# Kernel tuning notes

Hardware: AMD Instinct MI355X
Metric: run time of the kernel (lower is better)

Reference implementation:

```python
import jax, jax.numpy as jnp
import numpy as np

N_NODES = 100000
N_EDGES = 1600000
NFEAT, NHID, NCLASS = 128, 64, 40


def setup_inputs() -> dict:
    key = jax.random.key(0)
    k = jax.random.split(key, 6)
    x = jax.random.normal(k[0], (N_NODES, NFEAT), dtype=jnp.float32)
    edge_index = jax.random.randint(k[1], (2, N_EDGES), 0, N_NODES, dtype=jnp.int64)
    edge_weight = jax.random.uniform(k[2], (N_EDGES,), dtype=jnp.float32)
    # Glorot-style init as in PyG GCNConv.reset_parameters
    W1 = jax.random.normal(k[3], (NFEAT, NHID), dtype=jnp.float32) * (1.0 / np.sqrt(NFEAT))
    b1 = jnp.zeros((NHID,), dtype=jnp.float32)
    W2 = jax.random.normal(k[4], (NHID, NCLASS), dtype=jnp.float32) * (1.0 / np.sqrt(NHID))
    b2 = jnp.zeros((NCLASS,), dtype=jnp.float32)
    return {"x": x, "edge_index": edge_index, "edge_weight": edge_weight,
            "W1": W1, "b1": b1, "W2": W2, "b2": b2}


def _gcn_conv(x, edge_index, edge_weight, W, b):
    """PyG GCNConv: add self-loops, symmetric gcn_norm, linear, scatter-add, bias."""
    n = x.shape[0]
    loop = jnp.arange(n)
    row = jnp.concatenate([edge_index[0], loop])  # source nodes
    col = jnp.concatenate([edge_index[1], loop])  # target nodes
    w = jnp.concatenate([edge_weight, jnp.ones((n,), edge_weight.dtype)])
    deg = jax.ops.segment_sum(w, col, num_segments=n)          # [N]
    dinv = jnp.where(deg > 0, jax.lax.rsqrt(deg), 0.0)
    norm = dinv[row] * w * dinv[col]                           # [E+N]
    h = x @ W                                                  # [N, out]
    msg = norm[:, None] * h[row]                               # gather: [E+N, out]
    out = jax.ops.segment_sum(msg, col, num_segments=n)        # scatter-add: [N, out]
    return out + b


def reference(x, edge_index, edge_weight, W1, b1, W2, b2):
    h = jax.nn.relu(_gcn_conv(x, edge_index, edge_weight, W1, b1))
    # F.dropout with training=False is identity (eval mode)
    return _gcn_conv(h, edge_index, edge_weight, W2, b2)
```

## Files before the change

kernel.cpp:

```cpp
#include <hip/hip_runtime.h>
#include <hip/hip_bf16.h>

#define N_NODES 100000
#define N_EDGES 1600000
#define NFEAT 128
#define NHID 64
#define NCLASS 40
#define CAP 64

#define BIN_SHIFT 9
#define BIN_NODES 512
#define NBIN ((N_NODES + BIN_NODES - 1) / BIN_NODES)
#define SCAP 10240
#define CHUNK 4096
#define EPT 16

using frag_ab = __attribute__((ext_vector_type(8))) short;
using frag_cd = __attribute__((ext_vector_type(4))) float;


__device__ __forceinline__ unsigned pack2(float a, float b) {
    unsigned ua = __float_as_uint(a), ub = __float_as_uint(b);
    unsigned ra = (ua + 0x7FFFu + ((ua >> 16) & 1u)) >> 16;
    unsigned rb = (ub + 0x7FFFu + ((ub >> 16) & 1u)) >> 16;
    return ra | (rb << 16);
}
__device__ __forceinline__ unsigned short bf16rtn(float f) {
    unsigned u = __float_as_uint(f);
    return (unsigned short)((u + 0x7FFFu + ((u >> 16) & 1u)) >> 16);
}
__device__ __forceinline__ float lo16(unsigned w) { return __uint_as_float(w << 16); }
__device__ __forceinline__ float hi16(unsigned w) { return __uint_as_float(w & 0xFFFF0000u); }


__global__ __launch_bounds__(256) void bin_kernel(const int* __restrict__ ei,
                                                  const float* __restrict__ ew,
                                                  int* __restrict__ bincnt,
                                                  uint2* __restrict__ staging) {
    __shared__ int lcnt[NBIN];
    __shared__ int gbase[NBIN];
    int t = threadIdx.x;
    for (int i = t; i < NBIN; i += 256) lcnt[i] = 0;
    __syncthreads();

    int base = blockIdx.x * CHUNK;
    int c[EPT]; unsigned en[EPT];
#pragma unroll
    for (int u = 0; u < EPT; ++u) {
        int e = base + u * 256 + t;
        if (e < N_EDGES) {
            c[u] = ei[N_EDGES + e];
            unsigned wq = (unsigned)fminf(ew[e] * 32768.0f, 32767.0f);
            en[u] = ((unsigned)ei[e] << 15) | wq;
        } else {
            c[u] = -1;
        }
    }
#pragma unroll
    for (int u = 0; u < EPT; ++u)
        if (c[u] >= 0) atomicAdd(&lcnt[c[u] >> BIN_SHIFT], 1);
    __syncthreads();
    if (t < NBIN) {
        int n = lcnt[t];
        gbase[t] = (n > 0) ? atomicAdd(&bincnt[t], n) : 0;
    }
    __syncthreads();
    if (t < NBIN) lcnt[t] = 0;
    __syncthreads();
#pragma unroll
    for (int u = 0; u < EPT; ++u) {
        if (c[u] >= 0) {
            int b = c[u] >> BIN_SHIFT;
            int p = gbase[b] + atomicAdd(&lcnt[b], 1);
            if (p < SCAP)
                staging[(size_t)b * SCAP + p] = make_uint2(en[u], (unsigned)c[u]);
        }
    }
}


__global__ __launch_bounds__(512) void place_kernel(const int* __restrict__ bincnt,
                                                    const uint2* __restrict__ staging,
                                                    unsigned* __restrict__ bucket,
                                                    int* __restrict__ cnt,
                                                    float* __restrict__ dinv) {
    __shared__ int lpos[BIN_NODES];
    __shared__ float lws[BIN_NODES];
    int b = blockIdx.x;
    int t = threadIdx.x;
    for (int i = t; i < BIN_NODES; i += 512) { lpos[i] = 0; lws[i] = 0.0f; }
    __syncthreads();

    int nodebase = b << BIN_SHIFT;
    int n = bincnt[b];
    if (n > SCAP) n = SCAP;
    const uint2* st = staging + (size_t)b * SCAP;
    for (int i = t; i < n; i += 512) {
        uint2 en = st[i];
        int local = (int)en.y - nodebase;
        int p = atomicAdd(&lpos[local], 1);
        if (p < CAP) bucket[((size_t)en.y << 6) + p] = en.x;
        atomicAdd(&lws[local], (float)(en.x & 32767u) * (1.0f / 32768.0f));
    }
    __syncthreads();
    for (int i = t; i < BIN_NODES; i += 512) {
        int node = nodebase + i;
        if (node < N_NODES) {
            cnt[node] = min(lpos[i], CAP);
            dinv[node] = rsqrtf(1.0f + lws[i]);
        }
    }
}


__global__ __launch_bounds__(256) void prep_kernel(const float* __restrict__ W1,
                                                   const float* __restrict__ W2,
                                                   unsigned short* __restrict__ w1t,
                                                   unsigned short* __restrict__ w2t) {
    int idx = blockIdx.x * 256 + threadIdx.x;
    if (idx < NFEAT * NHID) {
        int k = idx >> 6, n = idx & 63;
        w1t[n * NFEAT + k] = bf16rtn(W1[idx]);
    }
    int idx2 = idx - NFEAT * NHID;
    if (idx2 >= 0 && idx2 < NHID * NCLASS) {
        int k = idx2 / NCLASS, n = idx2 - k * NCLASS;
        w2t[n * NHID + k] = bf16rtn(W2[idx2]);
    }
}


__global__ __launch_bounds__(256) void gemm1_kernel(const float* __restrict__ x,
                                                    const unsigned short* __restrict__ w1t,
                                                    unsigned short* __restrict__ h1b) {
    __shared__ unsigned short sm[16384];
    int t = threadIdx.x;
    int row0 = blockIdx.x * 64;

#pragma unroll
    for (int p = 0; p < 4; ++p) {
        int id = p * 256 + t;
        int r = id >> 4;
        int c = id & 15;
        int gr = row0 + r; if (gr > N_NODES - 1) gr = N_NODES - 1;
        const float* src = x + (size_t)gr * NFEAT + c * 8;
        float4 f0 = *(const float4*)src;
        float4 f1 = *(const float4*)(src + 4);
        uint4 pk = make_uint4(pack2(f0.x, f0.y), pack2(f0.z, f0.w),
                              pack2(f1.x, f1.y), pack2(f1.z, f1.w));
        int cs = c ^ (r & 15);
        *(uint4*)(&sm[r * 128 + cs * 8]) = pk;
    }
    const uint4* wt4 = (const uint4*)w1t;
#pragma unroll
    for (int p = 0; p < 4; ++p) {
        int id = p * 256 + t;
        int n = id >> 4;
        int c = id & 15;
        uint4 v = wt4[id];
        int cs = c ^ (n & 15);
        *(uint4*)(&sm[8192 + n * 128 + cs * 8]) = v;
    }
    __syncthreads();

    int w = t >> 6, l = t & 63;
    int li = l & 15, q = l >> 4;
    int arow = w * 16 + li;

    frag_cd acc0 = {0.f, 0.f, 0.f, 0.f};
    frag_cd acc1 = {0.f, 0.f, 0.f, 0.f};
    frag_cd acc2 = {0.f, 0.f, 0.f, 0.f};
    frag_cd acc3 = {0.f, 0.f, 0.f, 0.f};

#pragma unroll
    for (int kc = 0; kc < 4; ++kc) {
        int cc = (kc * 4 + q) ^ li;
        frag_ab a  = *(const frag_ab*)(&sm[arow * 128 + cc * 8]);
        frag_ab b0 = *(const frag_ab*)(&sm[8192 + (0 * 16 + li) * 128 + cc * 8]);
        frag_ab b1 = *(const frag_ab*)(&sm[8192 + (1 * 16 + li) * 128 + cc * 8]);
        frag_ab b2 = *(const frag_ab*)(&sm[8192 + (2 * 16 + li) * 128 + cc * 8]);
        frag_ab b3 = *(const frag_ab*)(&sm[8192 + (3 * 16 + li) * 128 + cc * 8]);
        acc0 = __builtin_amdgcn_mfma_f32_16x16x32_bf16(a, b0, acc0, 0, 0, 0);
        acc1 = __builtin_amdgcn_mfma_f32_16x16x32_bf16(a, b1, acc1, 0, 0, 0);
        acc2 = __builtin_amdgcn_mfma_f32_16x16x32_bf16(a, b2, acc2, 0, 0, 0);
        acc3 = __builtin_amdgcn_mfma_f32_16x16x32_bf16(a, b3, acc3, 0, 0, 0);
    }

#pragma unroll
    for (int reg = 0; reg < 4; ++reg) {
        int rrow = row0 + w * 16 + q * 4 + reg;
        if (rrow < N_NODES) {
            unsigned short* dst = h1b + (size_t)rrow * NHID + li;
            dst[0]  = bf16rtn(acc0[reg]);
            dst[16] = bf16rtn(acc1[reg]);
            dst[32] = bf16rtn(acc2[reg]);
            dst[48] = bf16rtn(acc3[reg]);
        }
    }
}


__global__ __launch_bounds__(256) void gather1_kernel(
        const int* __restrict__ cnt, const unsigned* __restrict__ bucket,
        const float* __restrict__ dinv, const unsigned short* __restrict__ h1b,
        const float* __restrict__ b1, unsigned short* __restrict__ relu1b) {
    int t = threadIdx.x;
    int lane = t & 63;
    int wave = t >> 6;
    int g = lane >> 3;
    int l = lane & 7;
    int node = (blockIdx.x * 4 + wave) * 8 + g;
    bool nvalid = node < N_NODES;
    int nd = nvalid ? node : N_NODES - 1;
    int d = cnt[nd];
    float dc = dinv[nd];

    uint4 eb0 = *(const uint4*)(bucket + ((size_t)nd << 6) + l * 8);
    uint4 eb1 = *(const uint4*)(bucket + ((size_t)nd << 6) + l * 8 + 4);
    int rl[8]; float wl[8];
#pragma unroll
    for (int k = 0; k < 8; ++k) {
        unsigned e = (k < 4) ? ((const unsigned*)&eb0)[k] : ((const unsigned*)&eb1)[k - 4];
        int slot = l * 8 + k;
        bool ok = slot < d;
        int r = ok ? (int)(e >> 15) : 0;
        rl[k] = r;
        wl[k] = ok ? (float)(e & 32767u) * (1.0f / 32768.0f) * dinv[r] : 0.0f;
    }

    uint4 hs = *(const uint4*)(h1b + (size_t)nd * NHID + l * 8);
    float acc[8];
#pragma unroll
    for (int k = 0; k < 4; ++k) {
        unsigned w = ((const unsigned*)&hs)[k];
        acc[2 * k] = dc * lo16(w);
        acc[2 * k + 1] = dc * hi16(w);
    }

    for (int j = 0; j < d; j += 8) {
        int src = (g << 3) + (j >> 3);
        int r[8]; float w[8];
#pragma unroll
        for (int k = 0; k < 8; ++k) { r[k] = __shfl(rl[k], src); w[k] = __shfl(wl[k], src); }
        uint4 v[8];
#pragma unroll
        for (int k = 0; k < 8; ++k)
            v[k] = *(const uint4*)(h1b + (size_t)r[k] * NHID + l * 8);
#pragma unroll
        for (int k = 0; k < 8; ++k) {
#pragma unroll
            for (int q = 0; q < 4; ++q) {
                unsigned ww = ((const unsigned*)&v[k])[q];
                acc[2 * q] += w[k] * lo16(ww);
                acc[2 * q + 1] += w[k] * hi16(ww);
            }
        }
    }
    if (nvalid) {
        float4 bv0 = *(const float4*)(b1 + l * 8);
        float4 bv1 = *(const float4*)(b1 + l * 8 + 4);
        float o0 = fmaxf(dc * acc[0] + bv0.x, 0.0f), o1 = fmaxf(dc * acc[1] + bv0.y, 0.0f);
        float o2 = fmaxf(dc * acc[2] + bv0.z, 0.0f), o3 = fmaxf(dc * acc[3] + bv0.w, 0.0f);
        float o4 = fmaxf(dc * acc[4] + bv1.x, 0.0f), o5 = fmaxf(dc * acc[5] + bv1.y, 0.0f);
        float o6 = fmaxf(dc * acc[6] + bv1.z, 0.0f), o7 = fmaxf(dc * acc[7] + bv1.w, 0.0f);
        uint4 pk = make_uint4(pack2(o0, o1), pack2(o2, o3), pack2(o4, o5), pack2(o6, o7));
        *(uint4*)(relu1b + (size_t)node * NHID + l * 8) = pk;
    }
}


__global__ __launch_bounds__(256) void gemm2_kernel(const unsigned short* __restrict__ relu1b,
                                                    const unsigned short* __restrict__ w2t,
                                                    unsigned short* __restrict__ h2b) {
    __shared__ unsigned short sa[64 * 64];
    __shared__ unsigned short sb[48 * 64];
    int t = threadIdx.x;
    int row0 = blockIdx.x * 64;

#pragma unroll
    for (int p = 0; p < 2; ++p) {
        int id = p * 256 + t;
        int r = id >> 3, cj = id & 7;
        int gr = row0 + r; if (gr > N_NODES - 1) gr = N_NODES - 1;
        uint4 v = *(const uint4*)(relu1b + (size_t)gr * NHID + cj * 8);
        int cs = cj ^ (r & 7);
        *(uint4*)(&sa[r * 64 + cs * 8]) = v;
    }
    for (int id = t; id < 384; id += 256) {
        int n = id >> 3, cj = id & 7;
        uint4 v = make_uint4(0u, 0u, 0u, 0u);
        if (n < NCLASS) v = *(const uint4*)(w2t + n * NHID + cj * 8);
        int cs = cj ^ (n & 7);
        *(uint4*)(&sb[n * 64 + cs * 8]) = v;
    }
    __syncthreads();

    int w = t >> 6, l = t & 63;
    int li = l & 15, q = l >> 4;
    int arow = w * 16 + li;

    frag_cd acc0 = {0.f, 0.f, 0.f, 0.f};
    frag_cd acc1 = {0.f, 0.f, 0.f, 0.f};
    frag_cd acc2 = {0.f, 0.f, 0.f, 0.f};

#pragma unroll
    for (int kc = 0; kc < 2; ++kc) {
        int cc = (kc * 4 + q) ^ (li & 7);
        frag_ab a  = *(const frag_ab*)(&sa[arow * 64 + cc * 8]);
        frag_ab b0 = *(const frag_ab*)(&sb[(0 + li) * 64 + cc * 8]);
        frag_ab b1 = *(const frag_ab*)(&sb[(16 + li) * 64 + cc * 8]);
        frag_ab b2 = *(const frag_ab*)(&sb[(32 + li) * 64 + cc * 8]);
        acc0 = __builtin_amdgcn_mfma_f32_16x16x32_bf16(a, b0, acc0, 0, 0, 0);
        acc1 = __builtin_amdgcn_mfma_f32_16x16x32_bf16(a, b1, acc1, 0, 0, 0);
        acc2 = __builtin_amdgcn_mfma_f32_16x16x32_bf16(a, b2, acc2, 0, 0, 0);
    }

#pragma unroll
    for (int reg = 0; reg < 4; ++reg) {
        int rrow = row0 + w * 16 + q * 4 + reg;
        if (rrow < N_NODES) {
            unsigned short* dst = h2b + (size_t)rrow * NCLASS;
            dst[li] = bf16rtn(acc0[reg]);
            dst[16 + li] = bf16rtn(acc1[reg]);
            if (li < 8) dst[32 + li] = bf16rtn(acc2[reg]);
        }
    }
}


__global__ __launch_bounds__(256) void gather2_kernel(
        const int* __restrict__ cnt, const unsigned* __restrict__ bucket,
        const float* __restrict__ dinv, const unsigned short* __restrict__ h2b,
        const float* __restrict__ b2, float* __restrict__ out) {
    int t = threadIdx.x;
    int lane = t & 63;
    int wave = t >> 6;
    int g = lane >> 4;
    int l = lane & 15;
    int node = (blockIdx.x * 4 + wave) * 4 + g;
    bool nvalid = node < N_NODES;
    int nd = nvalid ? node : N_NODES - 1;
    int d = cnt[nd];
    float dc = dinv[nd];
    bool fvalid = (l < 10);

    uint4 eb = *(const uint4*)(bucket + ((size_t)nd << 6) + l * 4);
    int rl[4]; float wl[4];
#pragma unroll
    for (int k = 0; k < 4; ++k) {
        unsigned e = ((const unsigned*)&eb)[k];
        int slot = l * 4 + k;
        bool ok = slot < d;
        int r = ok ? (int)(e >> 15) : 0;
        rl[k] = r;
        wl[k] = ok ? (float)(e & 32767u) * (1.0f / 32768.0f) * dinv[r] : 0.0f;
    }

    float acc[4] = {};
    int lc = fvalid ? l * 4 : 0;
    if (fvalid) {
        uint2 hs = *(const uint2*)(h2b + (size_t)nd * NCLASS + lc);
        acc[0] = dc * lo16(hs.x); acc[1] = dc * hi16(hs.x);
        acc[2] = dc * lo16(hs.y); acc[3] = dc * hi16(hs.y);
    }

    for (int j = 0; j < d; j += 4) {
        int src = (g << 4) + (j >> 2);
        int r0 = __shfl(rl[0], src), r1 = __shfl(rl[1], src);
        int r2 = __shfl(rl[2], src), r3 = __shfl(rl[3], src);
        float w0 = __shfl(wl[0], src), w1 = __shfl(wl[1], src);
        float w2 = __shfl(wl[2], src), w3 = __shfl(wl[3], src);
        if (fvalid) {
            uint2 v0 = *(const uint2*)(h2b + (size_t)r0 * NCLASS + lc);
            uint2 v1 = *(const uint2*)(h2b + (size_t)r1 * NCLASS + lc);
            uint2 v2 = *(const uint2*)(h2b + (size_t)r2 * NCLASS + lc);
            uint2 v3 = *(const uint2*)(h2b + (size_t)r3 * NCLASS + lc);
            acc[0] += w0 * lo16(v0.x) + w1 * lo16(v1.x) + w2 * lo16(v2.x) + w3 * lo16(v3.x);
            acc[1] += w0 * hi16(v0.x) + w1 * hi16(v1.x) + w2 * hi16(v2.x) + w3 * hi16(v3.x);
            acc[2] += w0 * lo16(v0.y) + w1 * lo16(v1.y) + w2 * lo16(v2.y) + w3 * lo16(v3.y);
            acc[3] += w0 * hi16(v0.y) + w1 * hi16(v1.y) + w2 * hi16(v2.y) + w3 * hi16(v3.y);
        }
    }
    if (nvalid && fvalid) {
        float4 bv = *(const float4*)(b2 + l * 4);
        *(float4*)(out + (size_t)node * NCLASS + l * 4) =
            make_float4(dc * acc[0] + bv.x, dc * acc[1] + bv.y,
                        dc * acc[2] + bv.z, dc * acc[3] + bv.w);
    }
}


extern "C" void kernel_launch(void* const* d_in, const int* in_sizes, int n_in,
                              void* d_out, int out_size, void* d_ws, size_t ws_size,
                              hipStream_t stream) {
    const float* x  = (const float*)d_in[0];
    const int*   ei = (const int*)d_in[1];
    const float* ew = (const float*)d_in[2];
    const float* W1 = (const float*)d_in[3];
    const float* b1 = (const float*)d_in[4];
    const float* W2 = (const float*)d_in[5];
    const float* b2 = (const float*)d_in[6];
    float* out = (float*)d_out;

    int*            bincnt  = (int*)d_ws;
    int*            cnt     = bincnt + 256;
    float*          dinv    = (float*)(cnt + 100352);
    unsigned*       bucket  = (unsigned*)(dinv + 100352);
    unsigned short* h1b     = (unsigned short*)(bucket + (size_t)N_NODES * CAP);
    unsigned short* region2 = h1b + (size_t)N_NODES * NHID;
    uint2*          staging = (uint2*)region2;
    unsigned short* relu1b  = region2;
    unsigned short* w1t     = region2 + (size_t)NBIN * SCAP * 4;
    unsigned short* w2t     = w1t + NFEAT * NHID;
    unsigned short* h2b     = h1b;

    hipMemsetAsync(bincnt, 0, NBIN * sizeof(int), stream);

    prep_kernel<<<42, 256, 0, stream>>>(W1, W2, w1t, w2t);
    bin_kernel<<<(N_EDGES + CHUNK - 1) / CHUNK, 256, 0, stream>>>(ei, ew, bincnt, staging);
    place_kernel<<<NBIN, 512, 0, stream>>>(bincnt, staging, bucket, cnt, dinv);

    gemm1_kernel<<<(N_NODES + 63) / 64, 256, 0, stream>>>(x, w1t, h1b);
    gather1_kernel<<<(N_NODES + 31) / 32, 256, 0, stream>>>(cnt, bucket, dinv, h1b, b1, relu1b);

    gemm2_kernel<<<(N_NODES + 63) / 64, 256, 0, stream>>>(relu1b, w2t, h2b);
    gather2_kernel<<<(N_NODES + 15) / 16, 256, 0, stream>>>(cnt, bucket, dinv, h2b, b2, out);
}
```

Baseline: 242.2 us.

## Fuse binning with GEMM1, drop weight prep, and degree-sort nodes for gathers

Merges the edge-binning and first GEMM into one launch split by block index so the two independent stages run concurrently. The weight-transpose prep kernel is removed and each GEMM block converts W1/W2 to bf16 directly. It also adds a per-degree histogram and a permutation kernel so the gather kernels process nodes grouped by degree, which should reduce wave divergence from uneven loop trip counts. In exchange there is an extra kernel, redundant per-block weight conversion, and scattered node access in the gathers that can cost locality.

```diff
diff --git a/kernel.cpp b/kernel.cpp
--- a/kernel.cpp
+++ b/kernel.cpp
@@ -14,6 +14,8 @@
 #define SCAP 10240
 #define CHUNK 4096
 #define EPT 16
+#define BIN_BLOCKS ((N_EDGES + CHUNK - 1) / CHUNK)
+#define GEMM1_BLOCKS ((N_NODES + 63) / 64)
 
 using frag_ab = __attribute__((ext_vector_type(8))) short;
 using frag_cd = __attribute__((ext_vector_type(4))) float;
@@ -33,109 +35,57 @@
 __device__ __forceinline__ float hi16(unsigned w) { return __uint_as_float(w & 0xFFFF0000u); }
 
 
-__global__ __launch_bounds__(256) void bin_kernel(const int* __restrict__ ei,
-                                                  const float* __restrict__ ew,
-                                                  int* __restrict__ bincnt,
-                                                  uint2* __restrict__ staging) {
-    __shared__ int lcnt[NBIN];
-    __shared__ int gbase[NBIN];
-    int t = threadIdx.x;
-    for (int i = t; i < NBIN; i += 256) lcnt[i] = 0;
-    __syncthreads();
-
-    int base = blockIdx.x * CHUNK;
-    int c[EPT]; unsigned en[EPT];
-#pragma unroll
-    for (int u = 0; u < EPT; ++u) {
-        int e = base + u * 256 + t;
-        if (e < N_EDGES) {
-            c[u] = ei[N_EDGES + e];
-            unsigned wq = (unsigned)fminf(ew[e] * 32768.0f, 32767.0f);
-            en[u] = ((unsigned)ei[e] << 15) | wq;
-        } else {
-            c[u] = -1;
-        }
-    }
-#pragma unroll
-    for (int u = 0; u < EPT; ++u)
-        if (c[u] >= 0) atomicAdd(&lcnt[c[u] >> BIN_SHIFT], 1);
-    __syncthreads();
-    if (t < NBIN) {
-        int n = lcnt[t];
-        gbase[t] = (n > 0) ? atomicAdd(&bincnt[t], n) : 0;
-    }
-    __syncthreads();
-    if (t < NBIN) lcnt[t] = 0;
-    __syncthreads();
-#pragma unroll
-    for (int u = 0; u < EPT; ++u) {
-        if (c[u] >= 0) {
-            int b = c[u] >> BIN_SHIFT;
-            int p = gbase[b] + atomicAdd(&lcnt[b], 1);
-            if (p < SCAP)
-                staging[(size_t)b * SCAP + p] = make_uint2(en[u], (unsigned)c[u]);
-        }
-    }
-}
-
-
-__global__ __launch_bounds__(512) void place_kernel(const int* __restrict__ bincnt,
-                                                    const uint2* __restrict__ staging,
-                                                    unsigned* __restrict__ bucket,
-                                                    int* __restrict__ cnt,
-                                                    float* __restrict__ dinv) {
-    __shared__ int lpos[BIN_NODES];
-    __shared__ float lws[BIN_NODES];
-    int b = blockIdx.x;
-    int t = threadIdx.x;
-    for (int i = t; i < BIN_NODES; i += 512) { lpos[i] = 0; lws[i] = 0.0f; }
-    __syncthreads();
-
-    int nodebase = b << BIN_SHIFT;
-    int n = bincnt[b];
-    if (n > SCAP) n = SCAP;
-    const uint2* st = staging + (size_t)b * SCAP;
-    for (int i = t; i < n; i += 512) {
-        uint2 en = st[i];
-        int local = (int)en.y - nodebase;
-        int p = atomicAdd(&lpos[local], 1);
-        if (p < CAP) bucket[((size_t)en.y << 6) + p] = en.x;
-        atomicAdd(&lws[local], (float)(en.x & 32767u) * (1.0f / 32768.0f));
-    }
-    __syncthreads();
-    for (int i = t; i < BIN_NODES; i += 512) {
-        int node = nodebase + i;
-        if (node < N_NODES) {
-            cnt[node] = min(lpos[i], CAP);
-            dinv[node] = rsqrtf(1.0f + lws[i]);
-        }
-    }
-}
-
-
-__global__ __launch_bounds__(256) void prep_kernel(const float* __restrict__ W1,
-                                                   const float* __restrict__ W2,
-                                                   unsigned short* __restrict__ w1t,
-                                                   unsigned short* __restrict__ w2t) {
-    int idx = blockIdx.x * 256 + threadIdx.x;
-    if (idx < NFEAT * NHID) {
-        int k = idx >> 6, n = idx & 63;
-        w1t[n * NFEAT + k] = bf16rtn(W1[idx]);
-    }
-    int idx2 = idx - NFEAT * NHID;
-    if (idx2 >= 0 && idx2 < NHID * NCLASS) {
-        int k = idx2 / NCLASS, n = idx2 - k * NCLASS;
-        w2t[n * NHID + k] = bf16rtn(W2[idx2]);
-    }
-}
-
-
-__global__ __launch_bounds__(256) void gemm1_kernel(const float* __restrict__ x,
-                                                    const unsigned short* __restrict__ w1t,
-                                                    unsigned short* __restrict__ h1b) {
+__global__ __launch_bounds__(256) void fusedA_kernel(
+        const int* __restrict__ ei, const float* __restrict__ ew,
+        int* __restrict__ bincnt, uint2* __restrict__ staging,
+        const float* __restrict__ x, const float* __restrict__ W1,
+        unsigned short* __restrict__ h1b) {
     __shared__ unsigned short sm[16384];
     int t = threadIdx.x;
-    int row0 = blockIdx.x * 64;
+
+    if (blockIdx.x < BIN_BLOCKS) {
+        int* lcnt  = (int*)sm;
+        int* gbase = lcnt + NBIN;
+        for (int i = t; i < NBIN; i += 256) lcnt[i] = 0;
+        __syncthreads();
+
+        int base = blockIdx.x * CHUNK;
+        int c[EPT]; unsigned en[EPT];
+#pragma unroll
+        for (int u = 0; u < EPT; ++u) {
+            int e = base + u * 256 + t;
+            if (e < N_EDGES) {
+                c[u] = ei[N_EDGES + e];
+                unsigned wq = (unsigned)fminf(ew[e] * 32768.0f, 32767.0f);
+                en[u] = ((unsigned)ei[e] << 15) | wq;
+            } else {
+                c[u] = -1;
+            }
+        }
+#pragma unroll
+        for (int u = 0; u < EPT; ++u)
+            if (c[u] >= 0) atomicAdd(&lcnt[c[u] >> BIN_SHIFT], 1);
+        __syncthreads();
+        if (t < NBIN) {
+            int n = lcnt[t];
+            gbase[t] = (n > 0) ? atomicAdd(&bincnt[t], n) : 0;
+        }
+        __syncthreads();
+        if (t < NBIN) lcnt[t] = 0;
+        __syncthreads();
+#pragma unroll
+        for (int u = 0; u < EPT; ++u) {
+            if (c[u] >= 0) {
+                int b = c[u] >> BIN_SHIFT;
+                int p = gbase[b] + atomicAdd(&lcnt[b], 1);
+                if (p < SCAP)
+                    staging[(size_t)b * SCAP + p] = make_uint2(en[u], (unsigned)c[u]);
+            }
+        }
+        return;
+    }
+
+    int row0 = (blockIdx.x - BIN_BLOCKS) * 64;
 
 #pragma unroll
     for (int p = 0; p < 4; ++p) {
@@ -151,15 +101,18 @@
         int cs = c ^ (r & 15);
         *(uint4*)(&sm[r * 128 + cs * 8]) = pk;
     }
-    const uint4* wt4 = (const uint4*)w1t;
 #pragma unroll
     for (int p = 0; p < 4; ++p) {
         int id = p * 256 + t;
         int n = id >> 4;
         int c = id & 15;
-        uint4 v = wt4[id];
+        const float* wsrc = W1 + (size_t)(c * 8) * NHID + n;
+        uint4 pk = make_uint4(pack2(wsrc[0 * NHID], wsrc[1 * NHID]),
+                              pack2(wsrc[2 * NHID], wsrc[3 * NHID]),
+                              pack2(wsrc[4 * NHID], wsrc[5 * NHID]),
+                              pack2(wsrc[6 * NHID], wsrc[7 * NHID]));
         int cs = c ^ (n & 15);
-        *(uint4*)(&sm[8192 + n * 128 + cs * 8]) = v;
+        *(uint4*)(&sm[8192 + n * 128 + cs * 8]) = pk;
     }
     __syncthreads();
 
@@ -200,35 +153,102 @@
 }
 
 
+__global__ __launch_bounds__(512) void place_kernel(const int* __restrict__ bincnt,
+                                                    const uint2* __restrict__ staging,
+                                                    unsigned* __restrict__ bucket,
+                                                    int* __restrict__ cnt,
+                                                    float* __restrict__ dinv,
+                                                    int* __restrict__ ghist) {
+    __shared__ int lpos[BIN_NODES];
+    __shared__ float lws[BIN_NODES];
+    __shared__ int lhist[CAP + 1];
+    int b = blockIdx.x;
+    int t = threadIdx.x;
+    for (int i = t; i < BIN_NODES; i += 512) { lpos[i] = 0; lws[i] = 0.0f; }
+    if (t <= CAP) lhist[t] = 0;
+    __syncthreads();
+
+    int nodebase = b << BIN_SHIFT;
+    int n = bincnt[b];
+    if (n > SCAP) n = SCAP;
+    const uint2* st = staging + (size_t)b * SCAP;
+    for (int i = t; i < n; i += 512) {
+        uint2 en = st[i];
+        int local = (int)en.y - nodebase;
+        int p = atomicAdd(&lpos[local], 1);
+        if (p < CAP) bucket[((size_t)en.y << 6) + p] = en.x;
+        atomicAdd(&lws[local], (float)(en.x & 32767u) * (1.0f / 32768.0f));
+    }
+    __syncthreads();
+    for (int i = t; i < BIN_NODES; i += 512) {
+        int node = nodebase + i;
+        if (node < N_NODES) {
+            int d = min(lpos[i], CAP);
+            cnt[node] = d;
+            dinv[node] = rsqrtf(1.0f + lws[i]);
+            atomicAdd(&lhist[d], 1);
+        }
+    }
+    __syncthreads();
+    if (t <= CAP) { int h = lhist[t]; if (h) atomicAdd(&ghist[t], h); }
+}
+
+
+__global__ __launch_bounds__(512) void perm_kernel(const int* __restrict__ cnt,
+                                                   const int* __restrict__ ghist,
+                                                   int* __restrict__ goffs,
+                                                   int* __restrict__ perm) {
+    __shared__ int base[CAP + 1];
+    __shared__ int lh[CAP + 1];
+    __shared__ int lbase[CAP + 1];
+    int t = threadIdx.x;
+    if (t <= CAP) lh[t] = 0;
+    if (t == 0) {
+        int s = 0;
+        for (int d = 0; d <= CAP; ++d) { base[d] = s; s += ghist[d]; }
+    }
+    __syncthreads();
+    int node = blockIdx.x * 512 + t;
+    bool v = node < N_NODES;
+    int d = 0, rank = 0;
+    if (v) { d = cnt[node]; rank = atomicAdd(&lh[d], 1); }
+    __syncthreads();
+    if (t <= CAP) { int h = lh[t]; lbase[t] = h ? atomicAdd(&goffs[t], h) : 0; }
+    __syncthreads();
+    if (v) perm[base[d] + lbase[d] + rank] = node;
+}
+
+
 __global__ __launch_bounds__(256) void gather1_kernel(
         const int* __restrict__ cnt, const unsigned* __restrict__ bucket,
         const float* __restrict__ dinv, const unsigned short* __restrict__ h1b,
-        const float* __restrict__ b1, unsigned short* __restrict__ relu1b) {
+        const float* __restrict__ b1, unsigned short* __restrict__ relu1b,
+        const int* __restrict__ perm) {
     int t = threadIdx.x;
     int lane = t & 63;
     int wave = t >> 6;
     int g = lane >> 3;
     int l = lane & 7;
-    int node = (blockIdx.x * 4 + wave) * 8 + g;
-    bool nvalid = node < N_NODES;
-    int nd = nvalid ? node : N_NODES - 1;
-    int d = cnt[nd];
-    float dc = dinv[nd];
-
-    uint4 eb0 = *(const uint4*)(bucket + ((size_t)nd << 6) + l * 8);
-    uint4 eb1 = *(const uint4*)(bucket + ((size_t)nd << 6) + l * 8 + 4);
+    int slot = (blockIdx.x * 4 + wave) * 8 + g;
+    bool nvalid = slot < N_NODES;
+    int node = perm[nvalid ? slot : 0];
+    int d = cnt[node];
+    float dc = dinv[node];
+
+    uint4 eb0 = *(const uint4*)(bucket + ((size_t)node << 6) + l * 8);
+    uint4 eb1 = *(const uint4*)(bucket + ((size_t)node << 6) + l * 8 + 4);
     int rl[8]; float wl[8];
 #pragma unroll
     for (int k = 0; k < 8; ++k) {
         unsigned e = (k < 4) ? ((const unsigned*)&eb0)[k] : ((const unsigned*)&eb1)[k - 4];
-        int slot = l * 8 + k;
-        bool ok = slot < d;
+        int sl = l * 8 + k;
+        bool ok = sl < d;
         int r = ok ? (int)(e >> 15) : 0;
         rl[k] = r;
         wl[k] = ok ? (float)(e & 32767u) * (1.0f / 32768.0f) * dinv[r] : 0.0f;
     }
 
-    uint4 hs = *(const uint4*)(h1b + (size_t)nd * NHID + l * 8);
+    uint4 hs = *(const uint4*)(h1b + (size_t)node * NHID + l * 8);
     float acc[8];
 #pragma unroll
     for (int k = 0; k < 4; ++k) {
@@ -270,7 +290,7 @@
 
 
 __global__ __launch_bounds__(256) void gemm2_kernel(const unsigned short* __restrict__ relu1b,
-                                                    const unsigned short* __restrict__ w2t,
+                                                    const float* __restrict__ W2,
                                                     unsigned short* __restrict__ h2b) {
     __shared__ unsigned short sa[64 * 64];
     __shared__ unsigned short sb[48 * 64];
@@ -289,7 +309,13 @@
     for (int id = t; id < 384; id += 256) {
         int n = id >> 3, cj = id & 7;
         uint4 v = make_uint4(0u, 0u, 0u, 0u);
-        if (n < NCLASS) v = *(const uint4*)(w2t + n * NHID + cj * 8);
+        if (n < NCLASS) {
+            const float* wsrc = W2 + (size_t)(cj * 8) * NCLASS + n;
+            v = make_uint4(pack2(wsrc[0 * NCLASS], wsrc[1 * NCLASS]),
+                           pack2(wsrc[2 * NCLASS], wsrc[3 * NCLASS]),
+                           pack2(wsrc[4 * NCLASS], wsrc[5 * NCLASS]),
+                           pack2(wsrc[6 * NCLASS], wsrc[7 * NCLASS]));
+        }
         int cs = cj ^ (n & 7);
         *(uint4*)(&sb[n * 64 + cs * 8]) = v;
     }
@@ -331,26 +357,27 @@
 __global__ __launch_bounds__(256) void gather2_kernel(
         const int* __restrict__ cnt, const unsigned* __restrict__ bucket,
         const float* __restrict__ dinv, const unsigned short* __restrict__ h2b,
-        const float* __restrict__ b2, float* __restrict__ out) {
+        const float* __restrict__ b2, float* __restrict__ out,
+        const int* __restrict__ perm) {
     int t = threadIdx.x;
     int lane = t & 63;
     int wave = t >> 6;
     int g = lane >> 4;
     int l = lane & 15;
-    int node = (blockIdx.x * 4 + wave) * 4 + g;
-    bool nvalid = node < N_NODES;
-    int nd = nvalid ? node : N_NODES - 1;
-    int d = cnt[nd];
-    float dc = dinv[nd];
+    int slot = (blockIdx.x * 4 + wave) * 4 + g;
+    bool nvalid = slot < N_NODES;
+    int node = perm[nvalid ? slot : 0];
+    int d = cnt[node];
+    float dc = dinv[node];
     bool fvalid = (l < 10);
 
-    uint4 eb = *(const uint4*)(bucket + ((size_t)nd << 6) + l * 4);
+    uint4 eb = *(const uint4*)(bucket + ((size_t)node << 6) + l * 4);
     int rl[4]; float wl[4];
 #pragma unroll
     for (int k = 0; k < 4; ++k) {
         unsigned e = ((const unsigned*)&eb)[k];
-        int slot = l * 4 + k;
-        bool ok = slot < d;
+        int sl = l * 4 + k;
+        bool ok = sl < d;
         int r = ok ? (int)(e >> 15) : 0;
         rl[k] = r;
         wl[k] = ok ? (float)(e & 32767u) * (1.0f / 32768.0f) * dinv[r] : 0.0f;
@@ -359,7 +386,7 @@
     float acc[4] = {};
     int lc = fvalid ? l * 4 : 0;
     if (fvalid) {
-        uint2 hs = *(const uint2*)(h2b + (size_t)nd * NCLASS + lc);
+        uint2 hs = *(const uint2*)(h2b + (size_t)node * NCLASS + lc);
         acc[0] = dc * lo16(hs.x); acc[1] = dc * hi16(hs.x);
         acc[2] = dc * lo16(hs.y); acc[3] = dc * hi16(hs.y);
     }
@@ -403,26 +430,29 @@
     float* out = (float*)d_out;
 
     int*            bincnt  = (int*)d_ws;
-    int*            cnt     = bincnt + 256;
+    int*            ghist   = bincnt + 256;
+    int*            goffs   = ghist + 65;
+    int*            cnt     = bincnt + 512;
     float*          dinv    = (float*)(cnt + 100352);
     unsigned*       bucket  = (unsigned*)(dinv + 100352);
     unsigned short* h1b     = (unsigned short*)(bucket + (size_t)N_NODES * CAP);
     unsigned short* region2 = h1b + (size_t)N_NODES * NHID;
     uint2*          staging = (uint2*)region2;
     unsigned short* relu1b  = region2;
-    unsigned short* w1t     = region2 + (size_t)NBIN * SCAP * 4;
-    unsigned short* w2t     = w1t + NFEAT * NHID;
+    int*            perm    = (int*)(relu1b + (size_t)N_NODES * NHID);
     unsigned short* h2b     = h1b;
 
-    hipMemsetAsync(bincnt, 0, NBIN * sizeof(int), stream);
-
-    prep_kernel<<<42, 256, 0, stream>>>(W1, W2, w1t, w2t);
-    bin_kernel<<<(N_EDGES + CHUNK - 1) / CHUNK, 256, 0, stream>>>(ei, ew, bincnt, staging);
-    place_kernel<<<NBIN, 512, 0, stream>>>(bincnt, staging, bucket, cnt, dinv);
-
-    gemm1_kernel<<<(N_NODES + 63) / 64, 256, 0, stream>>>(x, w1t, h1b);
-    gather1_kernel<<<(N_NODES + 31) / 32, 256, 0, stream>>>(cnt, bucket, dinv, h1b, b1, relu1b);
-
-    gemm2_kernel<<<(N_NODES + 63) / 64, 256, 0, stream>>>(relu1b, w2t, h2b);
-    gather2_kernel<<<(N_NODES + 15) / 16, 256, 0, stream>>>(cnt, bucket, dinv, h2b, b2, out);
-}
+    hipMemsetAsync(bincnt, 0, 512 * sizeof(int), stream);
+
+    fusedA_kernel<<<BIN_BLOCKS + GEMM1_BLOCKS, 256, 0, stream>>>(
+        ei, ew, bincnt, staging, x, W1, h1b);
+    place_kernel<<<NBIN, 512, 0, stream>>>(bincnt, staging, bucket, cnt, dinv, ghist);
+    perm_kernel<<<NBIN, 512, 0, stream>>>(cnt, ghist, goffs, perm);
+
+    gather1_kernel<<<(N_NODES + 31) / 32, 256, 0, stream>>>(
+        cnt, bucket, dinv, h1b, b1, relu1b, perm);
+
+    gemm2_kernel<<<(N_NODES + 63) / 64, 256, 0, stream>>>(relu1b, W2, h2b);
+    gather2_kernel<<<(N_NODES + 15) / 16, 256, 0, stream>>>(
+        cnt, bucket, dinv, h2b, b2, out, perm);
+}
```

After: 255.7 us. +5.6%, slower.

## Fold weight prep into GEMMs and software-pipeline neighbor gathers

Applied to the files above, without the earlier changes.

Removes the separate prep kernel: each GEMM block now reads the fp32 weights directly and packs them to bf16 while filling shared memory. Both gather kernels now prefetch the next batch of neighbor rows into registers while accumulating the current batch, so load latency overlaps with arithmetic. Bucket loads past the node's degree are skipped, and gather1 gets an occupancy hint in its launch bounds. The prefetch doubles the live register state, which may cut occupancy, and every GEMM block repeats the strided weight conversion.

```diff
diff --git a/kernel.cpp b/kernel.cpp
--- a/kernel.cpp
+++ b/kernel.cpp
@@ -113,25 +113,8 @@
 }
 
 
-__global__ __launch_bounds__(256) void prep_kernel(const float* __restrict__ W1,
-                                                   const float* __restrict__ W2,
-                                                   unsigned short* __restrict__ w1t,
-                                                   unsigned short* __restrict__ w2t) {
-    int idx = blockIdx.x * 256 + threadIdx.x;
-    if (idx < NFEAT * NHID) {
-        int k = idx >> 6, n = idx & 63;
-        w1t[n * NFEAT + k] = bf16rtn(W1[idx]);
-    }
-    int idx2 = idx - NFEAT * NHID;
-    if (idx2 >= 0 && idx2 < NHID * NCLASS) {
-        int k = idx2 / NCLASS, n = idx2 - k * NCLASS;
-        w2t[n * NHID + k] = bf16rtn(W2[idx2]);
-    }
-}
-
-
 __global__ __launch_bounds__(256) void gemm1_kernel(const float* __restrict__ x,
-                                                    const unsigned short* __restrict__ w1t,
+                                                    const float* __restrict__ W1,
                                                     unsigned short* __restrict__ h1b) {
     __shared__ unsigned short sm[16384];
     int t = threadIdx.x;
@@ -151,15 +134,18 @@
         int cs = c ^ (r & 15);
         *(uint4*)(&sm[r * 128 + cs * 8]) = pk;
     }
-    const uint4* wt4 = (const uint4*)w1t;
 #pragma unroll
     for (int p = 0; p < 4; ++p) {
         int id = p * 256 + t;
         int n = id >> 4;
         int c = id & 15;
-        uint4 v = wt4[id];
+        const float* wsrc = W1 + (size_t)(c * 8) * NHID + n;
+        uint4 pk = make_uint4(pack2(wsrc[0 * NHID], wsrc[1 * NHID]),
+                              pack2(wsrc[2 * NHID], wsrc[3 * NHID]),
+                              pack2(wsrc[4 * NHID], wsrc[5 * NHID]),
+                              pack2(wsrc[6 * NHID], wsrc[7 * NHID]));
         int cs = c ^ (n & 15);
-        *(uint4*)(&sm[8192 + n * 128 + cs * 8]) = v;
+        *(uint4*)(&sm[8192 + n * 128 + cs * 8]) = pk;
     }
     __syncthreads();
 
@@ -200,7 +186,7 @@
 }
 
 
-__global__ __launch_bounds__(256) void gather1_kernel(
+__global__ __launch_bounds__(256, 4) void gather1_kernel(
         const int* __restrict__ cnt, const unsigned* __restrict__ bucket,
         const float* __restrict__ dinv, const unsigned short* __restrict__ h1b,
         const float* __restrict__ b1, unsigned short* __restrict__ relu1b) {
@@ -215,14 +201,15 @@
     int d = cnt[nd];
     float dc = dinv[nd];
 
-    uint4 eb0 = *(const uint4*)(bucket + ((size_t)nd << 6) + l * 8);
-    uint4 eb1 = *(const uint4*)(bucket + ((size_t)nd << 6) + l * 8 + 4);
+    uint4 eb0 = make_uint4(0u, 0u, 0u, 0u), eb1 = make_uint4(0u, 0u, 0u, 0u);
+    if (l * 8 < d)     eb0 = *(const uint4*)(bucket + ((size_t)nd << 6) + l * 8);
+    if (l * 8 + 4 < d) eb1 = *(const uint4*)(bucket + ((size_t)nd << 6) + l * 8 + 4);
     int rl[8]; float wl[8];
 #pragma unroll
     for (int k = 0; k < 8; ++k) {
         unsigned e = (k < 4) ? ((const unsigned*)&eb0)[k] : ((const unsigned*)&eb1)[k - 4];
-        int slot = l * 8 + k;
-        bool ok = slot < d;
+        int sl = l * 8 + k;
+        bool ok = sl < d;
         int r = ok ? (int)(e >> 15) : 0;
         rl[k] = r;
         wl[k] = ok ? (float)(e & 32767u) * (1.0f / 32768.0f) * dinv[r] : 0.0f;
@@ -237,15 +224,28 @@
         acc[2 * k + 1] = dc * hi16(w);
     }
 
+    float w[8]; uint4 v[8];
+    if (d > 0) {
+        int src = g << 3;
+#pragma unroll
+        for (int k = 0; k < 8; ++k) {
+            int r = __shfl(rl[k], src);
+            w[k] = __shfl(wl[k], src);
+            v[k] = *(const uint4*)(h1b + (size_t)r * NHID + l * 8);
+        }
+    }
     for (int j = 0; j < d; j += 8) {
-        int src = (g << 3) + (j >> 3);
-        int r[8]; float w[8];
-#pragma unroll
-        for (int k = 0; k < 8; ++k) { r[k] = __shfl(rl[k], src); w[k] = __shfl(wl[k], src); }
-        uint4 v[8];
-#pragma unroll
-        for (int k = 0; k < 8; ++k)
-            v[k] = *(const uint4*)(h1b + (size_t)r[k] * NHID + l * 8);
+        bool more = (j + 8) < d;
+        float wn[8]; uint4 vn[8];
+        if (more) {
+            int src = (g << 3) + ((j + 8) >> 3);
+#pragma unroll
+            for (int k = 0; k < 8; ++k) {
+                int r = __shfl(rl[k], src);
+                wn[k] = __shfl(wl[k], src);
+                vn[k] = *(const uint4*)(h1b + (size_t)r * NHID + l * 8);
+            }
+        }
 #pragma unroll
         for (int k = 0; k < 8; ++k) {
 #pragma unroll
@@ -254,6 +254,10 @@
                 acc[2 * q] += w[k] * lo16(ww);
                 acc[2 * q + 1] += w[k] * hi16(ww);
             }
+        }
+        if (more) {
+#pragma unroll
+            for (int k = 0; k < 8; ++k) { w[k] = wn[k]; v[k] = vn[k]; }
         }
     }
     if (nvalid) {
@@ -270,7 +274,7 @@
 
 
 __global__ __launch_bounds__(256) void gemm2_kernel(const unsigned short* __restrict__ relu1b,
-                                                    const unsigned short* __restrict__ w2t,
+                                                    const float* __restrict__ W2,
                                                     unsigned short* __restrict__ h2b) {
     __shared__ unsigned short sa[64 * 64];
     __shared__ unsigned short sb[48 * 64];
@@ -289,7 +293,13 @@
     for (int id = t; id < 384; id += 256) {
         int n = id >> 3, cj = id & 7;
         uint4 v = make_uint4(0u, 0u, 0u, 0u);
-        if (n < NCLASS) v = *(const uint4*)(w2t + n * NHID + cj * 8);
+        if (n < NCLASS) {
+            const float* wsrc = W2 + (size_t)(cj * 8) * NCLASS + n;
+            v = make_uint4(pack2(wsrc[0 * NCLASS], wsrc[1 * NCLASS]),
+                           pack2(wsrc[2 * NCLASS], wsrc[3 * NCLASS]),
+                           pack2(wsrc[4 * NCLASS], wsrc[5 * NCLASS]),
+                           pack2(wsrc[6 * NCLASS], wsrc[7 * NCLASS]));
+        }
         int cs = cj ^ (n & 7);
         *(uint4*)(&sb[n * 64 + cs * 8]) = v;
     }
@@ -344,13 +354,14 @@
     float dc = dinv[nd];
     bool fvalid = (l < 10);
 
-    uint4 eb = *(const uint4*)(bucket + ((size_t)nd << 6) + l * 4);
+    uint4 eb = make_uint4(0u, 0u, 0u, 0u);
+    if (l * 4 < d) eb = *(const uint4*)(bucket + ((size_t)nd << 6) + l * 4);
     int rl[4]; float wl[4];
 #pragma unroll
     for (int k = 0; k < 4; ++k) {
         unsigned e = ((const unsigned*)&eb)[k];
-        int slot = l * 4 + k;
-        bool ok = slot < d;
+        int sl = l * 4 + k;
+        bool ok = sl < d;
         int r = ok ? (int)(e >> 15) : 0;
         rl[k] = r;
         wl[k] = ok ? (float)(e & 32767u) * (1.0f / 32768.0f) * dinv[r] : 0.0f;
@@ -364,21 +375,40 @@
         acc[2] = dc * lo16(hs.y); acc[3] = dc * hi16(hs.y);
     }
 
+    float w[4]; uint2 v[4];
+    if (d > 0) {
+        int src = g << 4;
+#pragma unroll
+        for (int k = 0; k < 4; ++k) {
+            int r = __shfl(rl[k], src);
+            w[k] = __shfl(wl[k], src);
+            if (fvalid) v[k] = *(const uint2*)(h2b + (size_t)r * NCLASS + lc);
+        }
+    }
     for (int j = 0; j < d; j += 4) {
-        int src = (g << 4) + (j >> 2);
-        int r0 = __shfl(rl[0], src), r1 = __shfl(rl[1], src);
-        int r2 = __shfl(rl[2], src), r3 = __shfl(rl[3], src);
-        float w0 = __shfl(wl[0], src), w1 = __shfl(wl[1], src);
-        float w2 = __shfl(wl[2], src), w3 = __shfl(wl[3], src);
+        bool more = (j + 4) < d;
+        float wn[4]; uint2 vn[4];
+        if (more) {
+            int src = (g << 4) + ((j + 4) >> 2);
+#pragma unroll
+            for (int k = 0; k < 4; ++k) {
+                int r = __shfl(rl[k], src);
+                wn[k] = __shfl(wl[k], src);
+                if (fvalid) vn[k] = *(const uint2*)(h2b + (size_t)r * NCLASS + lc);
+            }
+        }
         if (fvalid) {
-            uint2 v0 = *(const uint2*)(h2b + (size_t)r0 * NCLASS + lc);
-            uint2 v1 = *(const uint2*)(h2b + (size_t)r1 * NCLASS + lc);
-            uint2 v2 = *(const uint2*)(h2b + (size_t)r2 * NCLASS + lc);
-            uint2 v3 = *(const uint2*)(h2b + (size_t)r3 * NCLASS + lc);
-            acc[0] += w0 * lo16(v0.x) + w1 * lo16(v1.x) + w2 * lo16(v2.x) + w3 * lo16(v3.x);
-            acc[1] += w0 * hi16(v0.x) + w1 * hi16(v1.x) + w2 * hi16(v2.x) + w3 * hi16(v3.x);
-            acc[2] += w0 * lo16(v0.y) + w1 * lo16(v1.y) + w2 * lo16(v2.y) + w3 * lo16(v3.y);
-            acc[3] += w0 * hi16(v0.y) + w1 * hi16(v1.y) + w2 * hi16(v2.y) + w3 * hi16(v3.y);
+#pragma unroll
+            for (int k = 0; k < 4; ++k) {
+                acc[0] += w[k] * lo16(v[k].x);
+                acc[1] += w[k] * hi16(v[k].x);
+                acc[2] += w[k] * lo16(v[k].y);
+                acc[3] += w[k] * hi16(v[k].y);
+            }
+        }
+        if (more) {
+#pragma unroll
+            for (int k = 0; k < 4; ++k) { w[k] = wn[k]; v[k] = vn[k]; }
         }
     }
     if (nvalid && fvalid) {
@@ -410,19 +440,16 @@
     unsigned short* region2 = h1b + (size_t)N_NODES * NHID;
     uint2*          staging = (uint2*)region2;
     unsigned short* relu1b  = region2;
-    unsigned short* w1t     = region2 + (size_t)NBIN * SCAP * 4;
-    unsigned short* w2t     = w1t + NFEAT * NHID;
     unsigned short* h2b     = h1b;
 
-    hipMemsetAsync(bincnt, 0, NBIN * sizeof(int), stream);
-
-    prep_kernel<<<42, 256, 0, stream>>>(W1, W2, w1t, w2t);
+    hipMemsetAsync(bincnt, 0, 256 * sizeof(int), stream);
+
     bin_kernel<<<(N_EDGES + CHUNK - 1) / CHUNK, 256, 0, stream>>>(ei, ew, bincnt, staging);
     place_kernel<<<NBIN, 512, 0, stream>>>(bincnt, staging, bucket, cnt, dinv);
 
-    gemm1_kernel<<<(N_NODES + 63) / 64, 256, 0, stream>>>(x, w1t, h1b);
+    gemm1_kernel<<<(N_NODES + 63) / 64, 256, 0, stream>>>(x, W1, h1b);
     gather1_kernel<<<(N_NODES + 31) / 32, 256, 0, stream>>>(cnt, bucket, dinv, h1b, b1, relu1b);
 
-    gemm2_kernel<<<(N_NODES + 63) / 64, 256, 0, stream>>>(relu1b, w2t, h2b);
+    gemm2_kernel<<<(N_NODES + 63) / 64, 256, 0, stream>>>(relu1b, W2, h2b);
     gather2_kernel<<<(N_NODES + 15) / 16, 256, 0, stream>>>(cnt, bucket, dinv, h2b, b2, out);
 }
```

After: 351.9 us. 1.45x slower.
